# Kernel tuning notes

Hardware: AMD Instinct MI355X
Metric: run time of the kernel (lower is better)

Reference implementation:

```python
import jax, jax.numpy as jnp
import numpy as np

B, S, HID = 1, 2048, 2048
NH, HD, BS = 16, 128, 64
RATIO = 0.5
THETA = 10000.0


def rotate_half(x):
    h = x.shape[-1] // 2
    return jnp.concatenate([-x[..., h:], x[..., :h]], axis=-1)


def setup_inputs() -> dict:
    key = jax.random.key(0)
    ks = jax.random.split(key, 6)
    return {
        "hidden_states": jax.random.normal(ks[0], (B, S, HID), jnp.float32),
        "q_w": jax.random.normal(ks[1], (HID, NH * HD), jnp.float32) * 0.02,
        "k_w": jax.random.normal(ks[2], (HID, NH * HD), jnp.float32) * 0.02,
        "v_w": jax.random.normal(ks[3], (HID, NH * HD), jnp.float32) * 0.02,
        "o_w": jax.random.normal(ks[4], (NH * HD, HID), jnp.float32) * 0.02,
        # nn.init.uniform_(-0.1, 0.1)
        "sparsity_pattern": jax.random.uniform(ks[5], (NH, S // BS, S // BS), jnp.float32, -0.1, 0.1),
    }


def reference(hidden_states, q_w, k_w, v_w, o_w, sparsity_pattern):
    b, s, _ = hidden_states.shape
    # QKV projections (torch Linear: x @ W.T; here weights stored as [in, out])
    q = (hidden_states @ q_w).reshape(b, s, NH, HD).transpose(0, 2, 1, 3)  # [b,h,s,d]
    k = (hidden_states @ k_w).reshape(b, s, NH, HD).transpose(0, 2, 1, 3)
    v = (hidden_states @ v_w).reshape(b, s, NH, HD).transpose(0, 2, 1, 3)

    # RoPE (position_ids = arange)
    inv_freq = 1.0 / (THETA ** (jnp.arange(0, HD, 2, dtype=jnp.float32) / HD))
    pos = jnp.arange(s, dtype=jnp.float32)
    freqs = pos[:, None] * inv_freq[None, :]           # [s, d/2]
    emb = jnp.concatenate([freqs, freqs], axis=-1)     # [s, d]
    cos = jnp.cos(emb)[None, None].astype(q.dtype)     # [1,1,s,d]
    sin = jnp.sin(emb)[None, None].astype(q.dtype)
    q = q * cos + rotate_half(q) * sin
    k = k * cos + rotate_half(k) * sin

    # Learned per-head block-sparse mask via per-head top-k threshold
    nqb = s // BS  # 32
    kk = max(1, int(NH * nqb * nqb * RATIO / NH))  # 512
    flat = sparsity_pattern.reshape(NH, -1)
    top_vals, _ = jax.lax.top_k(flat, kk)
    thresh = top_vals[:, -1][:, None, None]
    block_mask = (sparsity_pattern > thresh).astype(jnp.float32)  # [h, nqb, nkb]
    # expand block mask to token resolution: [h, s, s]
    mask_full = jnp.repeat(jnp.repeat(block_mask, BS, axis=1), BS, axis=2)

    # scores: selected blocks get QK^T/sqrt(d), unselected blocks are exactly 0
    scores = jnp.einsum('bhqd,bhkd->bhqk', q, k) / np.sqrt(HD).astype(np.float32)
    scores = scores * mask_full[None]

    probs = jax.nn.softmax(scores.astype(jnp.float32), axis=-1).astype(q.dtype)
    attn = jnp.einsum('bhqk,bhkd->bhqd', probs, v)
    attn = attn.transpose(0, 2, 1, 3).reshape(b, s, NH * HD)
    return attn @ o_w
```

## Files before the change

kernel.cpp:

```cpp
#include <hip/hip_runtime.h>
#include <hip/hip_bf16.h>
#include <cstdint>
#include <cstddef>

typedef __bf16 bf16x8 __attribute__((ext_vector_type(8)));
typedef float f32x4 __attribute__((ext_vector_type(4)));
typedef unsigned short u16;

#define SEQ 2048
#define NH 16
#define HD 128
#define DMODEL 2048
#define NQKV 6144
#define NB 32
#define KSEL 512

__device__ __forceinline__ u16 f2bf(float f) {
  unsigned u = __float_as_uint(f);
  u += 0x7fffu + ((u >> 16) & 1u);
  return (u16)(u >> 16);
}
__device__ __forceinline__ float bf2f(u16 b) {
  return __uint_as_float(((unsigned)b) << 16);
}

__device__ __forceinline__ void async_copy16(const void* g, void* l) {
  __builtin_amdgcn_global_load_lds(
      (__attribute__((address_space(1))) void*)(unsigned long long)g,
      (__attribute__((address_space(3))) void*)(unsigned)(unsigned long long)l,
      16, 0, 0);
}

__global__ __launch_bounds__(256) void pre_kernel(
    const float* __restrict__ hidden, const float* __restrict__ qw,
    const float* __restrict__ kw, const float* __restrict__ vw,
    const float* __restrict__ ow, const float* __restrict__ sp,
    u16* __restrict__ Xb, u16* __restrict__ Wqkvt, u16* __restrict__ Wot,
    int* __restrict__ sel_cnt, int* __restrict__ sel_idx, unsigned* __restrict__ sel_mask,
    float2* __restrict__ sctab) {
  __shared__ __align__(16) char smem[64 * 65 * 4];
  int bid = blockIdx.x, t = threadIdx.x;
  if (bid < 16) {
    int h = bid;
    float* vals = (float*)smem;
    unsigned char* selb = (unsigned char*)(smem + 4096);
    for (int i = 0; i < 4; ++i) vals[t + i * 256] = sp[h * 1024 + t + i * 256];
    __syncthreads();
    for (int i = 0; i < 4; ++i) {
      float v = vals[t + i * 256];
      int cnt = 0;
      for (int j = 0; j < 1024; ++j) cnt += vals[j] > v ? 1 : 0;
      selb[t + i * 256] = (cnt < (KSEL - 1)) ? 1 : 0;
    }
    __syncthreads();
    if (t < NB) {
      int n = 0; unsigned m = 0;
      for (int kb = 0; kb < NB; ++kb) {
        if (selb[t * NB + kb]) { sel_idx[(h * NB + t) * NB + n] = kb; ++n; m |= 1u << kb; }
      }
      sel_cnt[h * NB + t] = n;
      sel_mask[h * NB + t] = m;
    }
    return;
  }
  if (bid < 32) {
    int b = bid - 16;
    for (int i = 0; i < 32; ++i) {
      int idx = i * 256 + t;
      int s = b * 128 + (idx >> 6), j = idx & 63;
      float inv = powf(10000.0f, -(float)j / 64.0f);
      float sn, cs;
      sincosf((float)s * inv, &sn, &cs);
      sctab[s * 64 + j] = make_float2(cs, sn);
    }
    return;
  }
  if (bid < 1056) {
    int base = (bid - 32) * 1024 + t;
    float4 v0 = ((const float4*)hidden)[base];
    float4 v1 = ((const float4*)hidden)[base + 256];
    float4 v2 = ((const float4*)hidden)[base + 512];
    float4 v3 = ((const float4*)hidden)[base + 768];
    ((ushort4*)Xb)[base]       = make_ushort4(f2bf(v0.x), f2bf(v0.y), f2bf(v0.z), f2bf(v0.w));
    ((ushort4*)Xb)[base + 256] = make_ushort4(f2bf(v1.x), f2bf(v1.y), f2bf(v1.z), f2bf(v1.w));
    ((ushort4*)Xb)[base + 512] = make_ushort4(f2bf(v2.x), f2bf(v2.y), f2bf(v2.z), f2bf(v2.w));
    ((ushort4*)Xb)[base + 768] = make_ushort4(f2bf(v3.x), f2bf(v3.y), f2bf(v3.z), f2bf(v3.w));
    return;
  }
  float(*tile)[65] = (float(*)[65])smem;
  for (int ti = 0; ti < 2; ++ti) {
    int tidx = (bid - 1056) * 2 + ti;
    int wsel = tidx >> 10, rem = tidx & 1023, bx = rem & 31, by = rem >> 5;
    const float* in = (wsel == 0) ? qw : (wsel == 1) ? kw : (wsel == 2) ? vw : ow;
    u16* out = (wsel == 3) ? Wot : Wqkvt + (size_t)wsel * DMODEL * 2048;
    int c0 = bx * 64, r0 = by * 64;
    if (ti) __syncthreads();
#pragma unroll
    for (int i = 0; i < 4; ++i) {
      int chunk = i * 256 + t, r = chunk >> 4, c4 = chunk & 15;
      float4 v = *(const float4*)(in + (size_t)(r0 + r) * 2048 + c0 + c4 * 4);
      tile[r][c4 * 4 + 0] = v.x; tile[r][c4 * 4 + 1] = v.y;
      tile[r][c4 * 4 + 2] = v.z; tile[r][c4 * 4 + 3] = v.w;
    }
    __syncthreads();
#pragma unroll
    for (int i = 0; i < 4; ++i) {
      int item = i * 256 + t, cc = item >> 4, rr4 = item & 15;
      ushort4 o = make_ushort4(f2bf(tile[rr4 * 4 + 0][cc]), f2bf(tile[rr4 * 4 + 1][cc]),
                               f2bf(tile[rr4 * 4 + 2][cc]), f2bf(tile[rr4 * 4 + 3][cc]));
      *(ushort4*)(out + (size_t)(c0 + cc) * 2048 + r0 + rr4 * 4) = o;
    }
  }
}

template <int MODE>
__global__ __launch_bounds__(256, 2) void gemm_bt_kernel(
    const u16* __restrict__ A, const u16* __restrict__ Bt, void* __restrict__ Cout,
    int M, int N, int K, const float2* __restrict__ sctab,
    u16* __restrict__ Qh, u16* __restrict__ Kh, u16* __restrict__ Vt,
    float* __restrict__ Vbsum) {
  __shared__ __align__(16) u16 As[8192];
  __shared__ __align__(16) u16 Bs[8192];
  const int t = threadIdx.x;
  const int lane = t & 63, w = t >> 6;
  const int wm = (w >> 1) * 64;
  const int quad = lane >> 4, l16 = lane & 15;
  const int m0 = blockIdx.y * 128, n0 = blockIdx.x * 128;
  const int ksplit = K / gridDim.z, kbeg = blockIdx.z * ksplit;

  f32x4 acc[4][4] = {};

  for (int kt = kbeg; kt < kbeg + ksplit; kt += 64) {
    __syncthreads();
#pragma unroll
    for (int j = 0; j < 4; ++j) {
      int sl = w * 256 + j * 64 + lane;
      int row = sl >> 3, c = (sl & 7) ^ (row & 7);
      const u16* ga = A + (size_t)(m0 + row) * K + kt + c * 8;
      const u16* gb = Bt + (size_t)(n0 + row) * K + kt + c * 8;
      async_copy16(ga, &As[(size_t)(w * 256 + j * 64) * 8]);
      async_copy16(gb, &Bs[(size_t)(w * 256 + j * 64) * 8]);
    }
    __syncthreads();
#pragma unroll
    for (int ks = 0; ks < 2; ++ks) {
      bf16x8 af[4], bfr[4];
#pragma unroll
      for (int mt = 0; mt < 4; ++mt) {
        int row = wm + mt * 16 + l16;
        af[mt] = *(const bf16x8*)(&As[(row * 8 + ((ks * 4 + quad) ^ (l16 & 7))) * 8]);
      }
#pragma unroll
      for (int nt = 0; nt < 4; ++nt) {
        int row = (w & 1) * 32 + (nt & 1) * 16 + (nt >> 1) * 64 + l16;
        bfr[nt] = *(const bf16x8*)(&Bs[(row * 8 + ((ks * 4 + quad) ^ (l16 & 7))) * 8]);
      }
#pragma unroll
      for (int mt = 0; mt < 4; ++mt)
#pragma unroll
        for (int nt = 0; nt < 4; ++nt)
          acc[mt][nt] = __builtin_amdgcn_mfma_f32_16x16x32_bf16(af[mt], bfr[nt], acc[mt][nt], 0, 0, 0);
    }
  }
  if (MODE < 2) {
#pragma unroll
    for (int mt = 0; mt < 4; ++mt)
#pragma unroll
      for (int nt = 0; nt < 4; ++nt) {
        int coff = n0 + (w & 1) * 32 + (nt & 1) * 16 + (nt >> 1) * 64 + l16;
#pragma unroll
        for (int p = 0; p < 4; ++p) {
          int row = m0 + wm + mt * 16 + quad * 4 + p;
          if (MODE == 0)
            ((float*)Cout)[(size_t)row * N + coff] = acc[mt][nt][p];
          else
            unsafeAtomicAdd(&((float*)Cout)[(size_t)row * N + coff], acc[mt][nt][p]);
        }
      }
    return;
  }
  int wsel = n0 >> 11;
  int h = (n0 >> 7) & 15;
  if (wsel < 2) {
    u16* dst = wsel ? Kh : Qh;
#pragma unroll
    for (int mt = 0; mt < 4; ++mt)
#pragma unroll
      for (int p = 0; p < 4; ++p) {
        int s = m0 + wm + mt * 16 + quad * 4 + p;
        const float2* trow = sctab + s * 64;
        u16* drow = dst + ((size_t)h * SEQ + s) * HD;
#pragma unroll
        for (int nt = 0; nt < 2; ++nt) {
          int j = (w & 1) * 32 + nt * 16 + l16;
          float2 cs = trow[j];
          float lo = acc[mt][nt][p], hi = acc[mt][nt + 2][p];
          drow[j]      = f2bf(lo * cs.x - hi * cs.y);
          drow[j + 64] = f2bf(hi * cs.x + lo * cs.y);
        }
      }
  } else {
    int sb = (m0 >> 6) + (wm >> 6);
#pragma unroll
    for (int nt = 0; nt < 4; ++nt) {
      int d = (w & 1) * 32 + (nt & 1) * 16 + (nt >> 1) * 64 + l16;
      u16* vrow = Vt + ((size_t)h * HD + d) * SEQ;
      float bsum = 0.f;
#pragma unroll
      for (int mt = 0; mt < 4; ++mt)
#pragma unroll
        for (int p = 0; p < 4; ++p) {
          int s = m0 + wm + mt * 16 + quad * 4 + p;
          float v = acc[mt][nt][p];
          vrow[s] = f2bf(v);
          bsum += v;
        }
      bsum += __shfl_xor(bsum, 16, 64);
      bsum += __shfl_xor(bsum, 32, 64);
      if (quad == 0) Vbsum[((size_t)h * NB + sb) * HD + d] = bsum;
    }
  }
}

__global__ __launch_bounds__(256, 2) void attn_kernel(
    const u16* __restrict__ Qh, const u16* __restrict__ Kh, const u16* __restrict__ Vt,
    const float* __restrict__ Vbsum, const int* __restrict__ sel_cnt,
    const int* __restrict__ sel_idx, const unsigned* __restrict__ sel_mask,
    u16* __restrict__ attnb) {
  __shared__ __align__(16) u16 Ks[2][8192];
  __shared__ __align__(16) u16 Vs[2][8192];
  __shared__ __align__(16) u16 pbuf[4][1024];
  int bid = blockIdx.x;
  int h = (bid & 7) * 2 + ((bid >> 3) >> 5);
  int qb = (bid >> 3) & 31;
  int t = threadIdx.x, lane = t & 63, w = t >> 6;
  int quad = lane >> 4, l16 = lane & 15;
  int rowblk = h * NB + qb;
  int nsel = sel_cnt[rowblk];
  unsigned smask = sel_mask[rowblk];
  const int* selrow = sel_idx + rowblk * NB;

  auto stageK = [&](int buf, int kb) {
    const u16* kbase = Kh + ((size_t)h * SEQ + kb * 64) * HD;
#pragma unroll
    for (int j = 0; j < 4; ++j) {
      int s = w * 256 + j * 64 + lane;
      int r = s >> 4, c = (s & 15) ^ (r & 15);
      async_copy16(kbase + (size_t)r * HD + c * 8, &Ks[buf][(w * 256 + j * 64) * 8]);
    }
  };
  auto stageV = [&](int buf, int kb) {
    const u16* vbase = Vt + (size_t)h * HD * SEQ + kb * 64;
#pragma unroll
    for (int j = 0; j < 4; ++j) {
      int s = w * 256 + j * 64 + lane;
      int d = s >> 3, c = (s & 7) ^ (d & 7);
      async_copy16(vbase + (size_t)d * SEQ + c * 8, &Vs[buf][(w * 256 + j * 64) * 8]);
    }
  };

  if (nsel > 0) { stageK(0, selrow[0]); stageV(0, selrow[0]); }

  float vc[8] = {};
  for (int kb = 0; kb < NB; ++kb)
    if (!((smask >> kb) & 1u)) {
      const float* vb = Vbsum + ((size_t)h * NB + kb) * HD + l16;
#pragma unroll
      for (int nt = 0; nt < 8; ++nt) vc[nt] += vb[nt * 16];
    }
  bf16x8 qf[4];
  {
    const u16* qbase = Qh + ((size_t)h * SEQ + qb * 64 + w * 16 + l16) * HD + quad * 8;
#pragma unroll
    for (int kk = 0; kk < 4; ++kk) qf[kk] = *(const bf16x8*)(qbase + kk * 32);
  }
  float rs[4] = {0.f, 0.f, 0.f, 0.f};
  f32x4 oacc[8] = {};
  const float scale = 0.08838834764831845f;
  u16* pb = pbuf[w];

  __syncthreads();

  for (int si = 0; si < nsel; ++si) {
    int cur = si & 1;
    if (si + 1 < nsel) {
      stageK(1 - cur, selrow[si + 1]);
      stageV(1 - cur, selrow[si + 1]);
    }

    f32x4 sacc[4] = {};
#pragma unroll
    for (int kk = 0; kk < 4; ++kk) {
#pragma unroll
      for (int nt = 0; nt < 4; ++nt) {
        int row = nt * 16 + l16;
        bf16x8 bfr = *(const bf16x8*)(&Ks[cur][(row * 16 + ((kk * 4 + quad) ^ l16)) * 8]);
        sacc[nt] = __builtin_amdgcn_mfma_f32_16x16x32_bf16(qf[kk], bfr, sacc[nt], 0, 0, 0);
      }
    }
#pragma unroll
    for (int nt = 0; nt < 4; ++nt) {
#pragma unroll
      for (int p = 0; p < 4; ++p) {
        float pv = __expf(sacc[nt][p] * scale);
        u16 pr = f2bf(pv);
        int row = quad * 4 + p, col = nt * 16 + l16;
        pb[row * 64 + (((col >> 3) ^ (row & 7)) << 3) + (col & 7)] = pr;
        rs[p] += bf2f(pr);
      }
    }
    asm volatile("s_waitcnt lgkmcnt(0)" ::: "memory");
#pragma unroll
    for (int ks2 = 0; ks2 < 2; ++ks2) {
      bf16x8 pf = *(const bf16x8*)(pb + l16 * 64 + (((ks2 * 4 + quad) ^ (l16 & 7)) << 3));
#pragma unroll
      for (int nt = 0; nt < 8; ++nt) {
        int d = nt * 16 + l16;
        bf16x8 vf = *(const bf16x8*)(&Vs[cur][(d * 8 + ((ks2 * 4 + quad) ^ (d & 7))) * 8]);
        oacc[nt] = __builtin_amdgcn_mfma_f32_16x16x32_bf16(pf, vf, oacc[nt], 0, 0, 0);
      }
    }
    __syncthreads();
  }
#pragma unroll
  for (int p = 0; p < 4; ++p)
#pragma unroll
    for (int off = 1; off < 16; off <<= 1)
      rs[p] += __shfl_xor(rs[p], off, 64);
  float cntm = (float)(64 * (NB - nsel));
#pragma unroll
  for (int p = 0; p < 4; ++p) {
    float inv = 1.0f / (rs[p] + cntm);
    int row = qb * 64 + w * 16 + quad * 4 + p;
#pragma unroll
    for (int nt = 0; nt < 8; ++nt) {
      float o = (oacc[nt][p] + vc[nt]) * inv;
      attnb[(size_t)row * DMODEL + h * HD + nt * 16 + l16] = f2bf(o);
    }
  }
}

extern "C" void kernel_launch(void* const* d_in, const int* in_sizes, int n_in,
                              void* d_out, int out_size, void* d_ws, size_t ws_size,
                              hipStream_t stream) {
  const float* hidden = (const float*)d_in[0];
  const float* q_w = (const float*)d_in[1];
  const float* k_w = (const float*)d_in[2];
  const float* v_w = (const float*)d_in[3];
  const float* o_w = (const float*)d_in[4];
  const float* sp  = (const float*)d_in[5];

  char* ws = (char*)d_ws;
  size_t off = 0;
  auto alloc = [&](size_t bytes) -> void* {
    void* p = ws + off;
    off += (bytes + 255) & ~(size_t)255;
    return p;
  };
  u16* Xb     = (u16*)alloc((size_t)SEQ * DMODEL * 2);
  u16* Wqkvt  = (u16*)alloc((size_t)NQKV * DMODEL * 2);
  u16* Wot    = (u16*)alloc((size_t)DMODEL * DMODEL * 2);
  u16* Qh     = (u16*)alloc((size_t)NH * SEQ * HD * 2);
  u16* Kh     = (u16*)alloc((size_t)NH * SEQ * HD * 2);
  u16* Vt     = (u16*)alloc((size_t)NH * HD * SEQ * 2);
  float* Vbsum = (float*)alloc((size_t)NH * NB * HD * 4);
  float2* sctab = (float2*)alloc((size_t)SEQ * 64 * 8);
  int* sel_cnt = (int*)alloc(NH * NB * 4);
  int* sel_idx = (int*)alloc(NH * NB * NB * 4);
  unsigned* sel_mask = (unsigned*)alloc(NH * NB * 4);
  u16* attnb = Xb;

  hipMemsetAsync(d_out, 0, (size_t)SEQ * DMODEL * 4, stream);

  pre_kernel<<<3104, 256, 0, stream>>>(hidden, q_w, k_w, v_w, o_w, sp,
                                       Xb, Wqkvt, Wot, sel_cnt, sel_idx, sel_mask, sctab);
  gemm_bt_kernel<2><<<dim3(NQKV / 128, SEQ / 128, 1), 256, 0, stream>>>(
      Xb, Wqkvt, nullptr, SEQ, NQKV, DMODEL, sctab, Qh, Kh, Vt, Vbsum);
  attn_kernel<<<512, 256, 0, stream>>>(Qh, Kh, Vt, Vbsum, sel_cnt, sel_idx,
                                       sel_mask, attnb);
  gemm_bt_kernel<1><<<dim3(DMODEL / 128, SEQ / 128, 2), 256, 0, stream>>>(
      attnb, Wot, d_out, SEQ, DMODEL, DMODEL, nullptr, nullptr, nullptr, nullptr, nullptr);
}
```

Baseline: 275.6 us.

## Split attention key blocks across two workgroups and add combine kernel

The attention kernel now launches twice as many workgroups. Each handles alternate selected key blocks for a query block and writes unnormalized fp32 partial outputs and row sums to scratch buffers, which reuse the QKV weight buffer and the output buffer. A new combine kernel adds the two partials and the contribution of the masked (zero-score) blocks, normalizes, and writes bf16. The K/V staging drops double buffering for a single buffer with two barriers per step, to cut LDS use and allow higher occupancy. The cost is extra fp32 traffic for the partials, an extra launch, and the output memset moved after the combine.

```diff
diff --git a/kernel.cpp b/kernel.cpp
--- a/kernel.cpp
+++ b/kernel.cpp
@@ -222,52 +222,44 @@
   }
 }
 
-__global__ __launch_bounds__(256, 2) void attn_kernel(
+__global__ __launch_bounds__(256, 4) void attn_kernel(
     const u16* __restrict__ Qh, const u16* __restrict__ Kh, const u16* __restrict__ Vt,
-    const float* __restrict__ Vbsum, const int* __restrict__ sel_cnt,
-    const int* __restrict__ sel_idx, const unsigned* __restrict__ sel_mask,
-    u16* __restrict__ attnb) {
-  __shared__ __align__(16) u16 Ks[2][8192];
-  __shared__ __align__(16) u16 Vs[2][8192];
+    const int* __restrict__ sel_cnt, const int* __restrict__ sel_idx,
+    float* __restrict__ O0, float* __restrict__ O1,
+    float* __restrict__ rs0, float* __restrict__ rs1) {
+  __shared__ __align__(16) u16 Ks[8192];
+  __shared__ __align__(16) u16 Vs[8192];
   __shared__ __align__(16) u16 pbuf[4][1024];
   int bid = blockIdx.x;
-  int h = (bid & 7) * 2 + ((bid >> 3) >> 5);
-  int qb = (bid >> 3) & 31;
+  int xcd = bid & 7, i = bid >> 3;
+  int half = i >> 6, j = i & 63;
+  int h = xcd * 2 + (j >> 5);
+  int qb = j & 31;
   int t = threadIdx.x, lane = t & 63, w = t >> 6;
   int quad = lane >> 4, l16 = lane & 15;
   int rowblk = h * NB + qb;
   int nsel = sel_cnt[rowblk];
-  unsigned smask = sel_mask[rowblk];
   const int* selrow = sel_idx + rowblk * NB;
 
-  auto stageK = [&](int buf, int kb) {
+  auto stageK = [&](int kb) {
     const u16* kbase = Kh + ((size_t)h * SEQ + kb * 64) * HD;
 #pragma unroll
-    for (int j = 0; j < 4; ++j) {
-      int s = w * 256 + j * 64 + lane;
+    for (int jj = 0; jj < 4; ++jj) {
+      int s = w * 256 + jj * 64 + lane;
       int r = s >> 4, c = (s & 15) ^ (r & 15);
-      async_copy16(kbase + (size_t)r * HD + c * 8, &Ks[buf][(w * 256 + j * 64) * 8]);
+      async_copy16(kbase + (size_t)r * HD + c * 8, &Ks[(w * 256 + jj * 64) * 8]);
     }
   };
-  auto stageV = [&](int buf, int kb) {
+  auto stageV = [&](int kb) {
     const u16* vbase = Vt + (size_t)h * HD * SEQ + kb * 64;
 #pragma unroll
-    for (int j = 0; j < 4; ++j) {
-      int s = w * 256 + j * 64 + lane;
+    for (int jj = 0; jj < 4; ++jj) {
+      int s = w * 256 + jj * 64 + lane;
       int d = s >> 3, c = (s & 7) ^ (d & 7);
-      async_copy16(vbase + (size_t)d * SEQ + c * 8, &Vs[buf][(w * 256 + j * 64) * 8]);
+      async_copy16(vbase + (size_t)d * SEQ + c * 8, &Vs[(w * 256 + jj * 64) * 8]);
     }
   };
 
-  if (nsel > 0) { stageK(0, selrow[0]); stageV(0, selrow[0]); }
-
-  float vc[8] = {};
-  for (int kb = 0; kb < NB; ++kb)
-    if (!((smask >> kb) & 1u)) {
-      const float* vb = Vbsum + ((size_t)h * NB + kb) * HD + l16;
-#pragma unroll
-      for (int nt = 0; nt < 8; ++nt) vc[nt] += vb[nt * 16];
-    }
   bf16x8 qf[4];
   {
     const u16* qbase = Qh + ((size_t)h * SEQ + qb * 64 + w * 16 + l16) * HD + quad * 8;
@@ -279,14 +271,12 @@
   const float scale = 0.08838834764831845f;
   u16* pb = pbuf[w];
 
-  __syncthreads();
-
-  for (int si = 0; si < nsel; ++si) {
-    int cur = si & 1;
-    if (si + 1 < nsel) {
-      stageK(1 - cur, selrow[si + 1]);
-      stageV(1 - cur, selrow[si + 1]);
-    }
+  for (int si = half; si < nsel; si += 2) {
+    int kb = selrow[si];
+    __syncthreads();
+    stageK(kb);
+    stageV(kb);
+    __syncthreads();
 
     f32x4 sacc[4] = {};
 #pragma unroll
@@ -294,7 +284,7 @@
 #pragma unroll
       for (int nt = 0; nt < 4; ++nt) {
         int row = nt * 16 + l16;
-        bf16x8 bfr = *(const bf16x8*)(&Ks[cur][(row * 16 + ((kk * 4 + quad) ^ l16)) * 8]);
+        bf16x8 bfr = *(const bf16x8*)(&Ks[(row * 16 + ((kk * 4 + quad) ^ l16)) * 8]);
         sacc[nt] = __builtin_amdgcn_mfma_f32_16x16x32_bf16(qf[kk], bfr, sacc[nt], 0, 0, 0);
       }
     }
@@ -316,27 +306,62 @@
 #pragma unroll
       for (int nt = 0; nt < 8; ++nt) {
         int d = nt * 16 + l16;
-        bf16x8 vf = *(const bf16x8*)(&Vs[cur][(d * 8 + ((ks2 * 4 + quad) ^ (d & 7))) * 8]);
+        bf16x8 vf = *(const bf16x8*)(&Vs[(d * 8 + ((ks2 * 4 + quad) ^ (d & 7))) * 8]);
         oacc[nt] = __builtin_amdgcn_mfma_f32_16x16x32_bf16(pf, vf, oacc[nt], 0, 0, 0);
       }
     }
-    __syncthreads();
   }
 #pragma unroll
   for (int p = 0; p < 4; ++p)
 #pragma unroll
     for (int off = 1; off < 16; off <<= 1)
       rs[p] += __shfl_xor(rs[p], off, 64);
-  float cntm = (float)(64 * (NB - nsel));
+  float* Ob = half ? O1 : O0;
+  float* rsb = half ? rs1 : rs0;
 #pragma unroll
   for (int p = 0; p < 4; ++p) {
-    float inv = 1.0f / (rs[p] + cntm);
     int row = qb * 64 + w * 16 + quad * 4 + p;
-#pragma unroll
-    for (int nt = 0; nt < 8; ++nt) {
-      float o = (oacc[nt][p] + vc[nt]) * inv;
-      attnb[(size_t)row * DMODEL + h * HD + nt * 16 + l16] = f2bf(o);
-    }
+    if (l16 == 0) rsb[h * SEQ + row] = rs[p];
+#pragma unroll
+    for (int nt = 0; nt < 8; ++nt)
+      Ob[(size_t)row * DMODEL + h * HD + nt * 16 + l16] = oacc[nt][p];
+  }
+}
+
+__global__ __launch_bounds__(256) void combine_kernel(
+    const float* __restrict__ O0, const float* __restrict__ O1,
+    const float* __restrict__ rs0, const float* __restrict__ rs1,
+    const float* __restrict__ Vbsum, const int* __restrict__ sel_cnt,
+    const unsigned* __restrict__ sel_mask, u16* __restrict__ attnb) {
+  __shared__ float vcs[HD];
+  __shared__ float rinv[64];
+  int sb = blockIdx.x, h = blockIdx.y, t = threadIdx.x;
+  int rowblk = h * NB + sb;
+  unsigned smask = sel_mask[rowblk];
+  float cntm = 64.0f * (float)(NB - sel_cnt[rowblk]);
+  if (t < HD) {
+    float c = 0.f;
+    for (int kb = 0; kb < NB; ++kb)
+      if (!((smask >> kb) & 1u)) c += Vbsum[((size_t)h * NB + kb) * HD + t];
+    vcs[t] = c;
+  } else if (t < HD + 64) {
+    int s = sb * 64 + (t - HD);
+    rinv[t - HD] = 1.0f / (rs0[h * SEQ + s] + rs1[h * SEQ + s] + cntm);
+  }
+  __syncthreads();
+#pragma unroll
+  for (int it = 0; it < 8; ++it) {
+    int idx = it * 256 + t;
+    int sl = idx >> 5, d4 = idx & 31;
+    size_t g = (size_t)(sb * 64 + sl) * DMODEL + h * HD + d4 * 4;
+    float4 a = *(const float4*)(O0 + g);
+    float4 b = *(const float4*)(O1 + g);
+    float iv = rinv[sl];
+    ushort4 o = make_ushort4(f2bf((a.x + b.x + vcs[d4 * 4 + 0]) * iv),
+                             f2bf((a.y + b.y + vcs[d4 * 4 + 1]) * iv),
+                             f2bf((a.z + b.z + vcs[d4 * 4 + 2]) * iv),
+                             f2bf((a.w + b.w + vcs[d4 * 4 + 3]) * iv));
+    *(ushort4*)(attnb + g) = o;
   }
 }
 
@@ -365,19 +390,23 @@
   u16* Vt     = (u16*)alloc((size_t)NH * HD * SEQ * 2);
   float* Vbsum = (float*)alloc((size_t)NH * NB * HD * 4);
   float2* sctab = (float2*)alloc((size_t)SEQ * 64 * 8);
+  float* rs0   = (float*)alloc((size_t)NH * SEQ * 4);
+  float* rs1   = (float*)alloc((size_t)NH * SEQ * 4);
   int* sel_cnt = (int*)alloc(NH * NB * 4);
   int* sel_idx = (int*)alloc(NH * NB * NB * 4);
   unsigned* sel_mask = (unsigned*)alloc(NH * NB * 4);
   u16* attnb = Xb;
-
-  hipMemsetAsync(d_out, 0, (size_t)SEQ * DMODEL * 4, stream);
+  float* O0 = (float*)Wqkvt;
+  float* O1 = (float*)d_out;
 
   pre_kernel<<<3104, 256, 0, stream>>>(hidden, q_w, k_w, v_w, o_w, sp,
                                        Xb, Wqkvt, Wot, sel_cnt, sel_idx, sel_mask, sctab);
   gemm_bt_kernel<2><<<dim3(NQKV / 128, SEQ / 128, 1), 256, 0, stream>>>(
       Xb, Wqkvt, nullptr, SEQ, NQKV, DMODEL, sctab, Qh, Kh, Vt, Vbsum);
-  attn_kernel<<<512, 256, 0, stream>>>(Qh, Kh, Vt, Vbsum, sel_cnt, sel_idx,
-                                       sel_mask, attnb);
+  attn_kernel<<<1024, 256, 0, stream>>>(Qh, Kh, Vt, sel_cnt, sel_idx, O0, O1, rs0, rs1);
+  combine_kernel<<<dim3(NB, NH), 256, 0, stream>>>(O0, O1, rs0, rs1, Vbsum,
+                                                   sel_cnt, sel_mask, attnb);
+  hipMemsetAsync(d_out, 0, (size_t)SEQ * DMODEL * 4, stream);
   gemm_bt_kernel<1><<<dim3(DMODEL / 128, SEQ / 128, 2), 256, 0, stream>>>(
       attnb, Wot, d_out, SEQ, DMODEL, DMODEL, nullptr, nullptr, nullptr, nullptr, nullptr);
 }
```

Measured after the change: 304.2 us. 10.4% more time.
